# Performance work log

Measured on AMD Instinct MI355X. Metric: run time of the kernel, lower is better.

Reference implementation:

```python
import jax, jax.numpy as jnp
import numpy as np
from jax import lax

B, C, H, W, K = 8, 128, 64, 64, 7
PAD = K // 2
TIMESTEPS = 8
BN_EPS = 1e-3


def _conv(x, w, pad):
    # x: [N,C,H,W], w: [O,I,kh,kw]
    return lax.conv_general_dilated(
        x, w, window_strides=(1, 1),
        padding=[(pad, pad), (pad, pad)],
        dimension_numbers=('NCHW', 'OIHW', 'NCHW'))


def _bn(x, g, b):
    # BatchNorm2d, track_running_stats=False -> always batch stats (biased var)
    m = jnp.mean(x, axis=(0, 2, 3), keepdims=True)
    v = jnp.var(x, axis=(0, 2, 3), keepdims=True)
    return (x - m) * lax.rsqrt(v + BN_EPS) * g[None, :, None, None] + b[None, :, None, None]


def _cb(b):
    return b[None, :, None, None]


def setup_inputs() -> dict:
    key = jax.random.key(0)
    ks = jax.random.split(key, 16)
    n = lambda k, sh, s=0.1: s * jax.random.normal(k, sh, dtype=jnp.float32)
    i_w_b = jax.random.uniform(ks[12], (C,), dtype=jnp.float32, minval=1.0, maxval=TIMESTEPS - 1.0)
    return {
        'input_': jax.random.normal(ks[0], (B, C, H, W), dtype=jnp.float32),
        'inhibition': jax.random.normal(ks[1], (B, C, H, W), dtype=jnp.float32),
        'excitation': jax.random.normal(ks[2], (B, C, H, W), dtype=jnp.float32),
        'a_w_w': n(ks[3], (1, C, K, K)), 'a_w_b': jnp.ones((1,), jnp.float32),
        'a_u_w': n(ks[4], (1, C, K, K)), 'a_u_b': jnp.ones((1,), jnp.float32),
        'i_w_w': n(ks[5], (C, C, 1, 1)), 'i_w_b': i_w_b,
        'i_u_w': n(ks[6], (C, C, 1, 1)), 'i_u_b': n(ks[7], (C,)),
        'e_w_w': n(ks[8], (C, C, 1, 1)), 'e_w_b': -i_w_b,
        'e_u_w': n(ks[9], (C, C, 1, 1)), 'e_u_b': n(ks[10], (C,)),
        'w_inh': n(ks[11], (C, C, K, K), 0.02),
        'w_exc': n(ks[13], (C, C, K, K), 0.02),
        'alpha': 0.1 * jnp.ones((C, 1, 1), jnp.float32),
        'gamma': jnp.ones((C, 1, 1), jnp.float32),
        'kappa': 0.5 * jnp.ones((C, 1, 1), jnp.float32),
        'w_param': 0.5 * jnp.ones((C, 1, 1), jnp.float32),
        'mu': jnp.ones((C, 1, 1), jnp.float32),
        'bn0_g': 0.1 * jnp.ones((C,), jnp.float32), 'bn0_b': jnp.zeros((C,), jnp.float32),
        'bn1_g': 0.1 * jnp.ones((C,), jnp.float32), 'bn1_b': jnp.zeros((C,), jnp.float32),
    }


def reference(input_, inhibition, excitation,
              a_w_w, a_w_b, a_u_w, a_u_b,
              i_w_w, i_w_b, i_u_w, i_u_b,
              e_w_w, e_w_b, e_u_w, e_u_b,
              w_inh, w_exc, alpha, gamma, kappa, w_param, mu,
              bn0_g, bn0_b, bn1_g, bn1_b):
    att_gate = jax.nn.sigmoid(_conv(input_, a_w_w, PAD) + _cb(a_w_b)
                              + _conv(excitation, a_u_w, PAD) + _cb(a_u_b))
    inh_intx = _bn(_conv(excitation * att_gate, w_inh, PAD), bn0_g, bn0_b)
    gated_inhibition = inhibition * att_gate
    gated_input = input_ * att_gate
    inhibition_hat = jnp.tanh(gated_input - jnp.tanh(inh_intx * (alpha * gated_inhibition + mu)))
    inh_gate = jax.nn.sigmoid(_conv(input_, i_w_w, 0) + _cb(i_w_b)
                              + _conv(inhibition, i_u_w, 0) + _cb(i_u_b))
    inhibition = (1.0 - inh_gate) * inhibition + inh_gate * inhibition_hat
    exc_gate = jax.nn.sigmoid(_conv(inhibition, e_w_w, 0) + _cb(e_w_b)
                              + _conv(excitation, e_u_w, 0) + _cb(e_u_b))
    exc_intx = _bn(_conv(inhibition, w_exc, PAD), bn1_g, bn1_b)
    excitation_hat = jnp.tanh(kappa * inhibition + gamma * exc_intx + w_param * inhibition * exc_intx)
    excitation = (1.0 - exc_gate) * excitation + exc_gate * excitation_hat
    return (inhibition, excitation)
```

## Files before the change

### kernel.cpp

```cpp
#include <hip/hip_runtime.h>
#include <cstddef>

typedef _Float16 f16;
typedef _Float16 f16x8 __attribute__((ext_vector_type(8)));
typedef float f32x16 __attribute__((ext_vector_type(16)));

#define Bc   8
#define Cc   128
#define Hc   64
#define Wc   64
#define HWc  4096
#define PADc 3
#define TAPS 49

#define PY 8
#define PX 16
#define WY 14
#define WX 22
#define NPOS (WY*WX)
#define AROW 256
#define ALDS_BYTES (NPOS*AROW)

__global__ __launch_bounds__(256) void prep_kernel(
    const float* __restrict__ w1, const float* __restrict__ w2,
    const float* __restrict__ iww, const float* __restrict__ iuw,
    const float* __restrict__ eww, const float* __restrict__ euw,
    f16* __restrict__ wt1, f16* __restrict__ wt2,
    f16* __restrict__ wgi, f16* __restrict__ wge,
    float* __restrict__ att)
{
    int idx = blockIdx.x*256 + threadIdx.x;
    const int NW = TAPS*Cc*Cc;
    if (idx < NW) {
        int tap = idx / (Cc*Cc);
        int rem = idx - tap*(Cc*Cc);
        int co = rem >> 7, ci = rem & 127;
        size_t src = (size_t)(co*Cc + ci)*TAPS + tap;
        wt1[idx] = (f16)w1[src];
        wt2[idx] = (f16)w2[src];
    }
    if (idx < 2*Cc*Cc) {
        int co = idx >> 8, k = idx & 255;
        wgi[idx] = (f16)((k < 128) ? iww[co*Cc + k] : iuw[co*Cc + (k-128)]);
        wge[idx] = (f16)((k < 128) ? eww[co*Cc + k] : euw[co*Cc + (k-128)]);
    }
    if (idx < Bc*HWc) att[idx] = 0.f;
}

__global__ __launch_bounds__(128) void att_partial(
    const float* __restrict__ input_, const float* __restrict__ exc,
    const float* __restrict__ aw, const float* __restrict__ au,
    float* __restrict__ att)
{
    __shared__ float wsa[32*49];
    __shared__ float wsb[32*49];
    __shared__ float ti[WY*WX];
    __shared__ float te[WY*WX];
    const int tid = threadIdx.x;
    const int tile = blockIdx.x;
    const int cch  = blockIdx.y*32;
    const int b    = blockIdx.z;
    for (int i = tid; i < 32*49; i += 128) { wsa[i] = aw[cch*49 + i]; wsb[i] = au[cch*49 + i]; }
    const int y0 = (tile >> 2)*8, x0 = (tile & 3)*16;
    const int tx = tid & 15, ty = tid >> 4;
    const float* ib = input_ + (size_t)b*Cc*HWc;
    const float* eb = exc    + (size_t)b*Cc*HWc;
    float acc = 0.f;
    for (int ci = 0; ci < 32; ++ci) {
        __syncthreads();
        for (int i = tid; i < WY*WX; i += 128) {
            int iy = i / WX, ix = i - iy*WX;
            int gy = y0 + iy - PADc, gx = x0 + ix - PADc;
            float v0 = 0.f, v1 = 0.f;
            if (gy >= 0 && gy < Hc && gx >= 0 && gx < Wc) {
                size_t o = (size_t)(cch+ci)*HWc + gy*Wc + gx;
                v0 = ib[o]; v1 = eb[o];
            }
            ti[i] = v0; te[i] = v1;
        }
        __syncthreads();
        const float* wa = &wsa[ci*49];
        const float* wb = &wsb[ci*49];
        #pragma unroll
        for (int kh = 0; kh < 7; ++kh) {
            #pragma unroll
            for (int kw = 0; kw < 7; ++kw) {
                const int k = kh*7+kw;
                acc += ti[(ty+kh)*WX + tx+kw] * wa[k];
                acc += te[(ty+kh)*WX + tx+kw] * wb[k];
            }
        }
    }
    atomicAdd(&att[(size_t)b*HWc + (size_t)(y0+ty)*Wc + (x0+tx)], acc);
}

__global__ __launch_bounds__(256) void att_final(
    float* __restrict__ att, const float* __restrict__ awb, const float* __restrict__ aub)
{
    int i = blockIdx.x*256 + threadIdx.x;
    float z = att[i] + awb[0] + aub[0];
    att[i] = 1.f/(1.f+expf(-z));
}

__global__ __launch_bounds__(256) void conv7_mfma(
    const float* __restrict__ x, const float* __restrict__ att,
    const f16* __restrict__ wt, float* __restrict__ out)
{
    __shared__ unsigned char smem[ALDS_BYTES];
    const int tid = threadIdx.x;
    const int x0 = blockIdx.x * PX;
    const int y0 = blockIdx.y * PY;
    const int b  = blockIdx.z;
    const float* xb = x + (size_t)b*Cc*HWc;

    for (int idx = tid; idx < NPOS*16; idx += 256) {
        int slot = idx / NPOS;
        int pos  = idx - slot*NPOS;
        int r = pos / WX, xw = pos - r*WX;
        int gy = y0 + r - PADc, gx = x0 + xw - PADc;
        bool inb = (gy >= 0 && gy < Hc && gx >= 0 && gx < Wc);
        float g = 1.f;
        if (att) g = inb ? att[(size_t)b*HWc + gy*Wc + gx] : 0.f;
        unsigned int pk[4];
        #pragma unroll
        for (int jj = 0; jj < 4; ++jj) {
            float v0 = 0.f, v1 = 0.f;
            if (inb) {
                size_t o = (size_t)(slot*8 + jj*2)*HWc + (size_t)gy*Wc + gx;
                v0 = xb[o]; v1 = xb[o + HWc];
            }
            f16 h0 = (f16)(v0*g), h1 = (f16)(v1*g);
            unsigned short u0 = __builtin_bit_cast(unsigned short, h0);
            unsigned short u1 = __builtin_bit_cast(unsigned short, h1);
            pk[jj] = (unsigned int)u0 | ((unsigned int)u1 << 16);
        }
        *(uint4*)(smem + pos*AROW + ((slot ^ (pos & 15)) << 4)) =
            make_uint4(pk[0], pk[1], pk[2], pk[3]);
    }
    __syncthreads();

    const int l   = tid & 63;
    const int wid = tid >> 6;
    const int wco = (wid >> 1) << 6;
    const int wpy = (wid & 1) << 2;
    const int lr  = l & 31;
    const int hi  = l >> 5;
    const int yA  = wpy + (lr >> 4);
    const int xA  = l & 15;

    f32x16 acc00 = {}, acc01 = {}, acc10 = {}, acc11 = {};

    const f16* wrow0 = wt + (size_t)(wco      + lr)*Cc + hi*8;
    const f16* wrow1 = wt + (size_t)(wco + 32 + lr)*Cc + hi*8;

    for (int t = 0; t < TAPS; ++t) {
        const int kh = t / 7, kw = t - kh*7;
        const int pos0 = (yA + kh)*WX + xA + kw;
        const int pos1 = pos0 + 2*WX;
        const size_t tapoff = (size_t)t*Cc*Cc;
        #pragma unroll
        for (int s = 0; s < 8; ++s) {
            const int slot = (s << 1) + hi;
            f16x8 a0 = *(const f16x8*)(wrow0 + tapoff + s*16);
            f16x8 a1 = *(const f16x8*)(wrow1 + tapoff + s*16);
            f16x8 b0 = *(const f16x8*)(smem + pos0*AROW + ((slot ^ (pos0 & 15)) << 4));
            f16x8 b1 = *(const f16x8*)(smem + pos1*AROW + ((slot ^ (pos1 & 15)) << 4));
            acc00 = __builtin_amdgcn_mfma_f32_32x32x16_f16(a0, b0, acc00, 0, 0, 0);
            acc01 = __builtin_amdgcn_mfma_f32_32x32x16_f16(a0, b1, acc01, 0, 0, 0);
            acc10 = __builtin_amdgcn_mfma_f32_32x32x16_f16(a1, b0, acc10, 0, 0, 0);
            acc11 = __builtin_amdgcn_mfma_f32_32x32x16_f16(a1, b1, acc11, 0, 0, 0);
        }
    }

    const int xg = x0 + xA;
    #pragma unroll
    for (int r = 0; r < 16; ++r) {
        const int cr = (r & 3) + 8*(r >> 2) + 4*hi;
        const int y00 = y0 + wpy + 0 + (lr >> 4);
        const int y01 = y0 + wpy + 2 + (lr >> 4);
        out[((size_t)b*Cc + wco      + cr)*HWc + (size_t)y00*Wc + xg] = acc00[r];
        out[((size_t)b*Cc + wco      + cr)*HWc + (size_t)y01*Wc + xg] = acc01[r];
        out[((size_t)b*Cc + wco + 32 + cr)*HWc + (size_t)y00*Wc + xg] = acc10[r];
        out[((size_t)b*Cc + wco + 32 + cr)*HWc + (size_t)y01*Wc + xg] = acc11[r];
    }
}

__global__ __launch_bounds__(256) void bn_stats_kernel(
    const float* __restrict__ x, const float* __restrict__ g,
    const float* __restrict__ bta, float* __restrict__ sc, float* __restrict__ bi)
{
    const int c = blockIdx.x;
    const int tid = threadIdx.x;
    float s = 0.f, s2 = 0.f;
    for (int i = tid; i < Bc*HWc; i += 256) {
        int b = i >> 12;
        int p = i & (HWc-1);
        float v = x[((size_t)b*Cc + c)*HWc + p];
        s += v; s2 += v*v;
    }
    #pragma unroll
    for (int off = 32; off > 0; off >>= 1) {
        s  += __shfl_down(s,  off);
        s2 += __shfl_down(s2, off);
    }
    __shared__ float ls[4], ls2[4];
    const int wv = tid >> 6;
    if ((tid & 63) == 0) { ls[wv] = s; ls2[wv] = s2; }
    __syncthreads();
    if (tid == 0) {
        s  = ls[0]+ls[1]+ls[2]+ls[3];
        s2 = ls2[0]+ls2[1]+ls2[2]+ls2[3];
        const float n = (float)(Bc*HWc);
        float m   = s / n;
        float var = s2 / n - m*m;
        float r   = rsqrtf(var + 1e-3f);
        float scale = r * g[c];
        sc[c] = scale;
        bi[c] = bta[c] - m*scale;
    }
}

__global__ __launch_bounds__(256) void gate_i_mfma(
    const float* __restrict__ input_, const float* __restrict__ inh,
    const f16* __restrict__ wg,
    const float* __restrict__ iwb, const float* __restrict__ uwb,
    const float* c1, const float* __restrict__ sc, const float* __restrict__ bi,
    const float* __restrict__ att,
    const float* __restrict__ alpha, const float* __restrict__ mu,
    float* out)
{
    __shared__ unsigned char bsm[128*512];
    __shared__ float sbias[Cc], ssc[Cc], sbi[Cc], sal[Cc], smu[Cc];
    const int tid = threadIdx.x;
    const int p0 = blockIdx.x * 128;
    const int b  = blockIdx.y;
    if (tid < Cc) {
        sbias[tid] = iwb[tid] + uwb[tid];
        ssc[tid] = sc[tid]; sbi[tid] = bi[tid];
        sal[tid] = alpha[tid]; smu[tid] = mu[tid];
    }
    const float* xb = input_ + (size_t)b*Cc*HWc + p0;
    const float* hb = inh    + (size_t)b*Cc*HWc + p0;
    #pragma unroll
    for (int it = 0; it < 16; ++it) {
        int idx = tid + it*256;
        int px = idx & 127, slot = idx >> 7;
        const float* src = (slot < 16) ? (xb + (size_t)(slot*8)*HWc)
                                       : (hb + (size_t)((slot-16)*8)*HWc);
        unsigned int pk[4];
        #pragma unroll
        for (int jj = 0; jj < 4; ++jj) {
            f16 h0 = (f16)src[(size_t)(jj*2  )*HWc + px];
            f16 h1 = (f16)src[(size_t)(jj*2+1)*HWc + px];
            pk[jj] = (unsigned)__builtin_bit_cast(unsigned short, h0)
                   | ((unsigned)__builtin_bit_cast(unsigned short, h1) << 16);
        }
        *(uint4*)(bsm + px*512 + ((slot ^ (px & 31)) << 4)) =
            make_uint4(pk[0], pk[1], pk[2], pk[3]);
    }
    __syncthreads();

    const int l   = tid & 63;
    const int wid = tid >> 6;
    const int wco = (wid >> 1) << 6;
    const int wpx = (wid & 1) << 6;
    const int lr  = l & 31;
    const int hi  = l >> 5;

    f32x16 acc00 = {}, acc01 = {}, acc10 = {}, acc11 = {};
    const f16* wr0 = wg + (size_t)(wco      + lr)*256 + hi*8;
    const f16* wr1 = wg + (size_t)(wco + 32 + lr)*256 + hi*8;
    const unsigned char* br0 = bsm + (size_t)(wpx      + lr)*512;
    const unsigned char* br1 = bsm + (size_t)(wpx + 32 + lr)*512;
    #pragma unroll
    for (int s = 0; s < 16; ++s) {
        const int slot = 2*s + hi;
        const int swz = (slot ^ lr) << 4;
        f16x8 a0 = *(const f16x8*)(wr0 + s*16);
        f16x8 a1 = *(const f16x8*)(wr1 + s*16);
        f16x8 b0 = *(const f16x8*)(br0 + swz);
        f16x8 b1 = *(const f16x8*)(br1 + swz);
        acc00 = __builtin_amdgcn_mfma_f32_32x32x16_f16(a0, b0, acc00, 0, 0, 0);
        acc01 = __builtin_amdgcn_mfma_f32_32x32x16_f16(a0, b1, acc01, 0, 0, 0);
        acc10 = __builtin_amdgcn_mfma_f32_32x32x16_f16(a1, b0, acc10, 0, 0, 0);
        acc11 = __builtin_amdgcn_mfma_f32_32x32x16_f16(a1, b1, acc11, 0, 0, 0);
    }

    const int pA = p0 + wpx + lr;
    const int pB = pA + 32;
    const float aA = att[(size_t)b*HWc + pA];
    const float aB = att[(size_t)b*HWc + pB];
    #pragma unroll
    for (int r = 0; r < 16; ++r) {
        const int cr = (r & 3) + 8*(r >> 2) + 4*hi;
        const int c0 = wco + cr, c1i = wco + 32 + cr;
        const float bz0 = sbias[c0], bz1 = sbias[c1i];
        const float sc0v = ssc[c0], sc1v = ssc[c1i];
        const float bi0v = sbi[c0], bi1v = sbi[c1i];
        const float al0 = sal[c0], al1 = sal[c1i];
        const float mu0 = smu[c0], mu1 = smu[c1i];
        #pragma unroll
        for (int q = 0; q < 4; ++q) {
            const int cc = (q < 2) ? c0 : c1i;
            const int pp = (q & 1) ? pB : pA;
            const float av = (q & 1) ? aB : aA;
            const float z = (q==0)?acc00[r]:(q==1)?acc01[r]:(q==2)?acc10[r]:acc11[r];
            const float bz = (q < 2) ? bz0 : bz1;
            const float scv = (q < 2) ? sc0v : sc1v;
            const float biv = (q < 2) ? bi0v : bi1v;
            const float alv = (q < 2) ? al0 : al1;
            const float muv = (q < 2) ? mu0 : mu1;
            size_t idx = ((size_t)b*Cc + cc)*HWc + pp;
            float hv = inh[idx];
            float xi = input_[idx];
            float intx = c1[idx]*scv + biv;
            float g = 1.f/(1.f+expf(-(z + bz)));
            float ihat = tanhf(xi*av - tanhf(intx*(alv*(hv*av) + muv)));
            out[idx] = (1.f-g)*hv + g*ihat;
        }
    }
}

__global__ __launch_bounds__(256) void gate_e_mfma(
    const float* __restrict__ hnew, const float* __restrict__ exc,
    const f16* __restrict__ wg,
    const float* __restrict__ ewb, const float* __restrict__ uwb,
    const float* c2, const float* __restrict__ sc, const float* __restrict__ bi,
    const float* __restrict__ kappa, const float* __restrict__ gamma_,
    const float* __restrict__ wp,
    float* out)
{
    __shared__ unsigned char bsm[128*512];
    __shared__ float sbias[Cc], ssc[Cc], sbi[Cc], skp[Cc], sgm[Cc], swp[Cc];
    const int tid = threadIdx.x;
    const int p0 = blockIdx.x * 128;
    const int b  = blockIdx.y;
    if (tid < Cc) {
        sbias[tid] = ewb[tid] + uwb[tid];
        ssc[tid] = sc[tid]; sbi[tid] = bi[tid];
        skp[tid] = kappa[tid]; sgm[tid] = gamma_[tid]; swp[tid] = wp[tid];
    }
    const float* xb = hnew + (size_t)b*Cc*HWc + p0;
    const float* eb = exc  + (size_t)b*Cc*HWc + p0;
    #pragma unroll
    for (int it = 0; it < 16; ++it) {
        int idx = tid + it*256;
        int px = idx & 127, slot = idx >> 7;
        const float* src = (slot < 16) ? (xb + (size_t)(slot*8)*HWc)
                                       : (eb + (size_t)((slot-16)*8)*HWc);
        unsigned int pk[4];
        #pragma unroll
        for (int jj = 0; jj < 4; ++jj) {
            f16 h0 = (f16)src[(size_t)(jj*2  )*HWc + px];
            f16 h1 = (f16)src[(size_t)(jj*2+1)*HWc + px];
            pk[jj] = (unsigned)__builtin_bit_cast(unsigned short, h0)
                   | ((unsigned)__builtin_bit_cast(unsigned short, h1) << 16);
        }
        *(uint4*)(bsm + px*512 + ((slot ^ (px & 31)) << 4)) =
            make_uint4(pk[0], pk[1], pk[2], pk[3]);
    }
    __syncthreads();

    const int l   = tid & 63;
    const int wid = tid >> 6;
    const int wco = (wid >> 1) << 6;
    const int wpx = (wid & 1) << 6;
    const int lr  = l & 31;
    const int hi  = l >> 5;

    f32x16 acc00 = {}, acc01 = {}, acc10 = {}, acc11 = {};
    const f16* wr0 = wg + (size_t)(wco      + lr)*256 + hi*8;
    const f16* wr1 = wg + (size_t)(wco + 32 + lr)*256 + hi*8;
    const unsigned char* br0 = bsm + (size_t)(wpx      + lr)*512;
    const unsigned char* br1 = bsm + (size_t)(wpx + 32 + lr)*512;
    #pragma unroll
    for (int s = 0; s < 16; ++s) {
        const int slot = 2*s + hi;
        const int swz = (slot ^ lr) << 4;
        f16x8 a0 = *(const f16x8*)(wr0 + s*16);
        f16x8 a1 = *(const f16x8*)(wr1 + s*16);
        f16x8 b0 = *(const f16x8*)(br0 + swz);
        f16x8 b1 = *(const f16x8*)(br1 + swz);
        acc00 = __builtin_amdgcn_mfma_f32_32x32x16_f16(a0, b0, acc00, 0, 0, 0);
        acc01 = __builtin_amdgcn_mfma_f32_32x32x16_f16(a0, b1, acc01, 0, 0, 0);
        acc10 = __builtin_amdgcn_mfma_f32_32x32x16_f16(a1, b0, acc10, 0, 0, 0);
        acc11 = __builtin_amdgcn_mfma_f32_32x32x16_f16(a1, b1, acc11, 0, 0, 0);
    }

    const int pA = p0 + wpx + lr;
    const int pB = pA + 32;
    #pragma unroll
    for (int r = 0; r < 16; ++r) {
        const int cr = (r & 3) + 8*(r >> 2) + 4*hi;
        const int c0 = wco + cr, c1i = wco + 32 + cr;
        #pragma unroll
        for (int q = 0; q < 4; ++q) {
            const int cc = (q < 2) ? c0 : c1i;
            const int pp = (q & 1) ? pB : pA;
            const float z = (q==0)?acc00[r]:(q==1)?acc01[r]:(q==2)?acc10[r]:acc11[r];
            size_t idx = ((size_t)b*Cc + cc)*HWc + pp;
            float hv = hnew[idx];
            float ev = exc[idx];
            float intx = c2[idx]*ssc[cc] + sbi[cc];
            float g = 1.f/(1.f+expf(-(z + sbias[cc])));
            float ehat = tanhf(skp[cc]*hv + sgm[cc]*intx + swp[cc]*hv*intx);
            out[idx] = (1.f-g)*ev + g*ehat;
        }
    }
}

extern "C" void kernel_launch(void* const* d_in, const int* in_sizes, int n_in,
                              void* d_out, int out_size, void* d_ws, size_t ws_size,
                              hipStream_t stream)
{
    (void)in_sizes; (void)n_in; (void)out_size; (void)ws_size;
    const float* input_ = (const float*)d_in[0];
    const float* inh    = (const float*)d_in[1];
    const float* exc    = (const float*)d_in[2];
    const float* a_w_w  = (const float*)d_in[3];
    const float* a_w_b  = (const float*)d_in[4];
    const float* a_u_w  = (const float*)d_in[5];
    const float* a_u_b  = (const float*)d_in[6];
    const float* i_w_w  = (const float*)d_in[7];
    const float* i_w_b  = (const float*)d_in[8];
    const float* i_u_w  = (const float*)d_in[9];
    const float* i_u_b  = (const float*)d_in[10];
    const float* e_w_w  = (const float*)d_in[11];
    const float* e_w_b  = (const float*)d_in[12];
    const float* e_u_w  = (const float*)d_in[13];
    const float* e_u_b  = (const float*)d_in[14];
    const float* w_inh  = (const float*)d_in[15];
    const float* w_exc  = (const float*)d_in[16];
    const float* alpha  = (const float*)d_in[17];
    const float* gamma_ = (const float*)d_in[18];
    const float* kappa  = (const float*)d_in[19];
    const float* w_par  = (const float*)d_in[20];
    const float* mu     = (const float*)d_in[21];
    const float* bn0_g  = (const float*)d_in[22];
    const float* bn0_b  = (const float*)d_in[23];
    const float* bn1_g  = (const float*)d_in[24];
    const float* bn1_b  = (const float*)d_in[25];

    float* out = (float*)d_out;
    const size_t N = (size_t)Bc*Cc*HWc;
    float* c1 = out;
    float* c2 = out + N;

    float* att = (float*)d_ws;
    float* sc0 = att + 32768;
    float* bi0 = sc0 + Cc;
    float* sc1 = bi0 + Cc;
    float* bi1 = sc1 + Cc;
    f16* wt1 = (f16*)((char*)d_ws + 33280u*4u);
    f16* wt2 = wt1 + (size_t)TAPS*Cc*Cc;
    f16* wgi = wt2 + (size_t)TAPS*Cc*Cc;
    f16* wge = wgi + 2*Cc*Cc;

    prep_kernel<<<(TAPS*Cc*Cc + 255)/256, 256, 0, stream>>>(
        w_inh, w_exc, i_w_w, i_u_w, e_w_w, e_u_w, wt1, wt2, wgi, wge, att);
    att_partial<<<dim3(32, 4, Bc), 128, 0, stream>>>(input_, exc, a_w_w, a_u_w, att);
    att_final<<<(Bc*HWc)/256, 256, 0, stream>>>(att, a_w_b, a_u_b);
    conv7_mfma<<<dim3(4, 8, Bc), 256, 0, stream>>>(exc, att, wt1, c1);
    bn_stats_kernel<<<Cc, 256, 0, stream>>>(c1, bn0_g, bn0_b, sc0, bi0);
    gate_i_mfma<<<dim3(HWc/128, Bc), 256, 0, stream>>>(
        input_, inh, wgi, i_w_b, i_u_b, c1, sc0, bi0, att, alpha, mu, out);
    conv7_mfma<<<dim3(4, 8, Bc), 256, 0, stream>>>(out, nullptr, wt2, c2);
    bn_stats_kernel<<<Cc, 256, 0, stream>>>(c2, bn1_g, bn1_b, sc1, bi1);
    gate_e_mfma<<<dim3(HWc/128, Bc), 256, 0, stream>>>(
        out, exc, wge, e_w_b, e_u_b, c2, sc1, bi1, kappa, gamma_, w_par, out + N);
}
```

Baseline: 640.8 us.

## Split conv7 output channels across two blocks and double-buffer weight loads

Each conv7 block now computes only half of the output channels (64 instead of 128), so the grid doubles and each wave holds two accumulators instead of four. The per-tap weight fragments are prefetched into registers one tap ahead (ping-pong buffers), so global loads overlap the MFMAs. This raises occupancy and parallelism. The cost is that each block still stages the full input tile into LDS, so the fp32-to-fp16 staging work and global reads of activations are duplicated across the two halves.

```diff
diff --git a/kernel.cpp b/kernel.cpp
--- a/kernel.cpp
+++ b/kernel.cpp
@@ -109,7 +109,8 @@
     __shared__ unsigned char smem[ALDS_BYTES];
     const int tid = threadIdx.x;
     const int x0 = blockIdx.x * PX;
-    const int y0 = blockIdx.y * PY;
+    const int y0 = (blockIdx.y >> 1) * PY;
+    const int cohalf = (blockIdx.y & 1) * 64;
     const int b  = blockIdx.z;
     const float* xb = x + (size_t)b*Cc*HWc;
 
@@ -141,47 +142,58 @@
 
     const int l   = tid & 63;
     const int wid = tid >> 6;
-    const int wco = (wid >> 1) << 6;
+    const int wco = cohalf + ((wid >> 1) << 5);
     const int wpy = (wid & 1) << 2;
     const int lr  = l & 31;
     const int hi  = l >> 5;
     const int yA  = wpy + (lr >> 4);
     const int xA  = l & 15;
 
-    f32x16 acc00 = {}, acc01 = {}, acc10 = {}, acc11 = {};
-
-    const f16* wrow0 = wt + (size_t)(wco      + lr)*Cc + hi*8;
-    const f16* wrow1 = wt + (size_t)(wco + 32 + lr)*Cc + hi*8;
-
-    for (int t = 0; t < TAPS; ++t) {
-        const int kh = t / 7, kw = t - kh*7;
-        const int pos0 = (yA + kh)*WX + xA + kw;
-        const int pos1 = pos0 + 2*WX;
-        const size_t tapoff = (size_t)t*Cc*Cc;
-        #pragma unroll
-        for (int s = 0; s < 8; ++s) {
-            const int slot = (s << 1) + hi;
-            f16x8 a0 = *(const f16x8*)(wrow0 + tapoff + s*16);
-            f16x8 a1 = *(const f16x8*)(wrow1 + tapoff + s*16);
-            f16x8 b0 = *(const f16x8*)(smem + pos0*AROW + ((slot ^ (pos0 & 15)) << 4));
-            f16x8 b1 = *(const f16x8*)(smem + pos1*AROW + ((slot ^ (pos1 & 15)) << 4));
-            acc00 = __builtin_amdgcn_mfma_f32_32x32x16_f16(a0, b0, acc00, 0, 0, 0);
-            acc01 = __builtin_amdgcn_mfma_f32_32x32x16_f16(a0, b1, acc01, 0, 0, 0);
-            acc10 = __builtin_amdgcn_mfma_f32_32x32x16_f16(a1, b0, acc10, 0, 0, 0);
-            acc11 = __builtin_amdgcn_mfma_f32_32x32x16_f16(a1, b1, acc11, 0, 0, 0);
-        }
-    }
+    f32x16 acc00 = {}, acc01 = {};
+
+    const f16* wrow = wt + (size_t)(wco + lr)*Cc + hi*8;
+
+#define LOADW(buf, t) { \
+        const f16* _p = wrow + (size_t)(t)*Cc*Cc; \
+        _Pragma("unroll") \
+        for (int _s = 0; _s < 8; ++_s) buf[_s] = *(const f16x8*)(_p + _s*16); \
+    }
+
+#define MFMA_TAP(buf, t) { \
+        const int _kh = (t)/7, _kw = (t) - _kh*7; \
+        const int _pos0 = (yA + _kh)*WX + xA + _kw; \
+        const int _pos1 = _pos0 + 2*WX; \
+        _Pragma("unroll") \
+        for (int _s = 0; _s < 8; ++_s) { \
+            const int _slot = (_s << 1) + hi; \
+            f16x8 _b0 = *(const f16x8*)(smem + _pos0*AROW + ((_slot ^ (_pos0 & 15)) << 4)); \
+            f16x8 _b1 = *(const f16x8*)(smem + _pos1*AROW + ((_slot ^ (_pos1 & 15)) << 4)); \
+            acc00 = __builtin_amdgcn_mfma_f32_32x32x16_f16(buf[_s], _b0, acc00, 0, 0, 0); \
+            acc01 = __builtin_amdgcn_mfma_f32_32x32x16_f16(buf[_s], _b1, acc01, 0, 0, 0); \
+        } \
+    }
+
+    f16x8 bufA[8], bufB[8];
+    LOADW(bufA, 0)
+    for (int t = 0; t < TAPS-1; t += 2) {
+        LOADW(bufB, t+1)
+        MFMA_TAP(bufA, t)
+        if (t+2 < TAPS) LOADW(bufA, t+2)
+        MFMA_TAP(bufB, t+1)
+    }
+    MFMA_TAP(bufA, TAPS-1)
+
+#undef LOADW
+#undef MFMA_TAP
 
     const int xg = x0 + xA;
     #pragma unroll
     for (int r = 0; r < 16; ++r) {
         const int cr = (r & 3) + 8*(r >> 2) + 4*hi;
-        const int y00 = y0 + wpy + 0 + (lr >> 4);
-        const int y01 = y0 + wpy + 2 + (lr >> 4);
-        out[((size_t)b*Cc + wco      + cr)*HWc + (size_t)y00*Wc + xg] = acc00[r];
-        out[((size_t)b*Cc + wco      + cr)*HWc + (size_t)y01*Wc + xg] = acc01[r];
-        out[((size_t)b*Cc + wco + 32 + cr)*HWc + (size_t)y00*Wc + xg] = acc10[r];
-        out[((size_t)b*Cc + wco + 32 + cr)*HWc + (size_t)y01*Wc + xg] = acc11[r];
+        const int y00 = y0 + wpy + (lr >> 4);
+        const int y01 = y00 + 2;
+        out[((size_t)b*Cc + wco + cr)*HWc + (size_t)y00*Wc + xg] = acc00[r];
+        out[((size_t)b*Cc + wco + cr)*HWc + (size_t)y01*Wc + xg] = acc01[r];
     }
 }
 
@@ -460,11 +472,11 @@
         w_inh, w_exc, i_w_w, i_u_w, e_w_w, e_u_w, wt1, wt2, wgi, wge, att);
     att_partial<<<dim3(32, 4, Bc), 128, 0, stream>>>(input_, exc, a_w_w, a_u_w, att);
     att_final<<<(Bc*HWc)/256, 256, 0, stream>>>(att, a_w_b, a_u_b);
-    conv7_mfma<<<dim3(4, 8, Bc), 256, 0, stream>>>(exc, att, wt1, c1);
+    conv7_mfma<<<dim3(4, 16, Bc), 256, 0, stream>>>(exc, att, wt1, c1);
     bn_stats_kernel<<<Cc, 256, 0, stream>>>(c1, bn0_g, bn0_b, sc0, bi0);
     gate_i_mfma<<<dim3(HWc/128, Bc), 256, 0, stream>>>(
         input_, inh, wgi, i_w_b, i_u_b, c1, sc0, bi0, att, alpha, mu, out);
-    conv7_mfma<<<dim3(4, 8, Bc), 256, 0, stream>>>(out, nullptr, wt2, c2);
+    conv7_mfma<<<dim3(4, 16, Bc), 256, 0, stream>>>(out, nullptr, wt2, c2);
     bn_stats_kernel<<<Cc, 256, 0, stream>>>(c2, bn1_g, bn1_b, sc1, bi1);
     gate_e_mfma<<<dim3(HWc/128, Bc), 256, 0, stream>>>(
         out, exc, wge, e_w_b, e_u_b, c2, sc1, bi1, kappa, gamma_, w_par, out + N);
```

Result: slower. 767.9 us (+19.8%).
